# Performance work log

Measured on AMD Instinct MI355X. Metric: run time of the kernel, lower is better.

The kernel has to match this reference:

```python
import jax, jax.numpy as jnp
import numpy as np

B, S, D = 4, 4096, 1024
G, N, BLK, K = 8, 64, 8, 4
GD = D // G
NL = 24


def setup_inputs() -> dict:
    key = jax.random.key(0)
    ks = jax.random.split(key, 16)
    f32 = jnp.float32
    rn = lambda k, sh, s: jax.random.normal(k, sh, f32) * s
    inp = {}
    inp["x_r"] = jax.random.normal(ks[0], (B, S, D), f32)
    inp["x_i"] = jax.random.normal(ks[1], (B, S, D), f32)
    inp["norm_w"] = jnp.ones((D,), f32)
    inp["sg_theta"] = rn(ks[2], (D // BLK,), 0.1)
    inp["sg_Wg"] = rn(ks[3], (D, D), 1.0 / np.sqrt(D))
    inp["sg_bg"] = jnp.zeros((D,), f32)
    inp["conv_w"] = rn(ks[4], (2 * D, 2, K), 1.0 / np.sqrt(2 * K))
    inp["conv_b"] = jnp.zeros((2 * D,), f32)
    inp["log_A_mag"] = jax.random.uniform(ks[5], (G, N), f32) * 0.5 + 0.5
    inp["A_phase"] = rn(ks[6], (G, N), 0.1)
    inp["B_Wr"] = rn(ks[7], (N, GD), 1.0 / np.sqrt(GD))
    inp["B_Wi"] = rn(ks[8], (N, GD), 1.0 / np.sqrt(GD))
    inp["C_Wr"] = rn(ks[9], (GD, N), 1.0 / np.sqrt(N))
    inp["C_Wi"] = rn(ks[10], (GD, N), 1.0 / np.sqrt(N))
    inp["dt_W"] = rn(ks[11], (2, 2 * GD), 1.0 / np.sqrt(2 * GD))
    inp["dt_b"] = jnp.zeros((2,), f32)
    inp["out_Wr"] = rn(ks[12], (D, D), 1.0 / np.sqrt(D))
    inp["out_Wi"] = rn(ks[13], (D, D), 1.0 / np.sqrt(D))
    inp["act_thr"] = jnp.zeros((), f32)
    inp["ssm_scale"] = jnp.full((D,), 2.5, f32)
    inp["res_scale"] = jnp.asarray(1.0 / np.sqrt(2.0 * NL), f32)
    return inp


def reference(x_r, x_i, norm_w, sg_theta, sg_Wg, sg_bg, conv_w, conv_b,
              log_A_mag, A_phase, B_Wr, B_Wi, C_Wr, C_Wi, dt_W, dt_b,
              out_Wr, out_Wi, act_thr, ssm_scale, res_scale):
    b, s, d = x_r.shape
    g, n, gd = G, N, GD
    # --- ComplexRMSNorm: normalize by RMS of complex magnitude ---
    inv = jax.lax.rsqrt(jnp.mean(x_r * x_r + x_i * x_i, axis=-1, keepdims=True) + 1e-6)
    xr = x_r * inv * norm_w
    xi = x_i * inv * norm_w
    # --- SpinorGate: block-diagonal phase rotation with selective sigmoid gate ---
    theta = jnp.repeat(sg_theta, BLK)  # per-block angle broadcast to [D]
    mag = jnp.sqrt(xr * xr + xi * xi + 1e-8)
    gate = jax.nn.sigmoid(jnp.einsum('bsd,ed->bse', mag, sg_Wg) + sg_bg)
    ct, st = jnp.cos(theta), jnp.sin(theta)
    xr, xi = gate * (xr * ct - xi * st), gate * (xr * st + xi * ct)
    # --- grouped causal conv over interleaved real/imag channels ---
    x_il = jnp.stack([xr, xi], axis=-1).reshape(b, s, 2 * d).transpose(0, 2, 1)  # [B,2D,S]
    x_il = jnp.pad(x_il, ((0, 0), (0, 0), (K - 1, 0)))  # causal left pad
    co = jax.lax.conv_general_dilated(
        x_il, conv_w, (1,), 'VALID',
        dimension_numbers=('NCH', 'OIH', 'NCH'), feature_group_count=d)
    co = co + conv_b[None, :, None]
    co = co.transpose(0, 2, 1).reshape(b, s, d, 2)
    xr, xi = co[..., 0], co[..., 1]
    # --- magnitude-gated activation ---
    act = 1.0 - jnp.exp(-(xr * xr + xi * xi) * jnp.exp(act_thr))
    xr = xr * act
    xi = xi * act
    # --- MIMO groups ---
    xgr = xr.reshape(b, s, g, gd)
    xgi = xi.reshape(b, s, g, gd)
    # --- selective dt from concatenated real/imag features ---
    xcat = jnp.concatenate([xgr, xgi], axis=-1)  # [B,S,G,2*gd]
    dt = jnp.clip(jnp.exp(jnp.einsum('bsgd,ed->bsge', xcat, dt_W) + dt_b), 1e-4, 2.0)
    dt_mag, dt_ph = dt[..., 0:1], dt[..., 1:2]
    # --- discretized complex A (|A| < 1 guaranteed) ---
    a_mag = jnp.exp(dt_mag * (-jax.nn.softplus(log_A_mag)))  # [B,S,G,N]
    ang = dt_ph * A_phase
    ar = a_mag * jnp.cos(ang)
    ai = a_mag * jnp.sin(ang)
    # --- complex B projection ---
    bxr = (jnp.einsum('bsgd,nd->bsgn', xgr, B_Wr)
           - jnp.einsum('bsgd,nd->bsgn', xgi, B_Wi)) * dt_mag
    bxi = (jnp.einsum('bsgd,nd->bsgn', xgr, B_Wi)
           + jnp.einsum('bsgd,nd->bsgn', xgi, B_Wr)) * dt_mag
    # --- complex selective scan with renorm every 256 steps ---
    def step(carry, inp):
        hr, hi = carry
        a_r, a_i, b_r, b_i, t = inp
        nhr = a_r * hr - a_i * hi + b_r
        nhi = a_r * hi + a_i * hr + b_i
        hn = jnp.sqrt(nhr * nhr + nhi * nhi + 1e-8)
        sc = jnp.where((t + 1) % 256 == 0, jnp.minimum(hn, 100.0) / hn, 1.0)
        nhr = nhr * sc
        nhi = nhi * sc
        return (nhr, nhi), (nhr, nhi)

    h0 = jnp.zeros((b, g, n), x_r.dtype)
    mv = lambda a: jnp.moveaxis(a, 1, 0)  # [S,B,G,N]
    _, (Hr, Hi) = jax.lax.scan(step, (h0, h0),
                               (mv(ar), mv(ai), mv(bxr), mv(bxi), jnp.arange(s)))
    Hr = jnp.moveaxis(Hr, 0, 1)  # [B,S,G,N]
    Hi = jnp.moveaxis(Hi, 0, 1)
    # --- complex C projection ---
    yr = (jnp.einsum('bsgn,dn->bsgd', Hr, C_Wr)
          - jnp.einsum('bsgn,dn->bsgd', Hi, C_Wi)).reshape(b, s, d)
    yi = (jnp.einsum('bsgn,dn->bsgd', Hr, C_Wi)
          + jnp.einsum('bsgn,dn->bsgd', Hi, C_Wr)).reshape(b, s, d)
    # --- complex output projection, real per-channel scale, residual ---
    o_r = (jnp.einsum('bsd,ed->bse', yr, out_Wr)
           - jnp.einsum('bsd,ed->bse', yi, out_Wi)) * ssm_scale
    o_i = (jnp.einsum('bsd,ed->bse', yr, out_Wi)
           + jnp.einsum('bsd,ed->bse', yi, out_Wr)) * ssm_scale
    return jnp.stack([x_r + res_scale * o_r, x_i + res_scale * o_i], axis=-1)
```

## Files before the change

### kernel.cpp

```cpp
#include <hip/hip_runtime.h>
#include <hip/hip_bf16.h>
#include <hip/hip_fp8.h>
#include <math.h>

#define BB 4
#define SS 4096
#define DD 1024
#define GG 8
#define NN 64
#define GDIM 128
#define BS (BB*SS)
static const size_t BSD  = (size_t)BS * DD;
static const size_t BSGN = (size_t)BS * GG * NN;

typedef __attribute__((ext_vector_type(8))) short bf16x8;
typedef __attribute__((ext_vector_type(4))) float f32x4;
typedef __attribute__((ext_vector_type(4))) uint u32x4;
typedef unsigned char uchar;

__device__ inline ushort f2b(float x) {
    __hip_bfloat16 h = __float2bfloat16(x);
    return *reinterpret_cast<ushort*>(&h);
}
__device__ inline float b2f(ushort u) {
    union { uint q; float f; } x; x.q = ((uint)u) << 16; return x.f;
}
__device__ inline uchar f2fp8(float x) {
    __hip_fp8_e4m3 h(x);
    return *reinterpret_cast<uchar*>(&h);
}
__device__ __forceinline__ bf16x8 neg8(bf16x8 v) {
    union { bf16x8 b; u32x4 u; } x;
    x.b = v;
    x.u ^= 0x80008000u;
    return x.b;
}

#define GL16(gp, lp) __builtin_amdgcn_global_load_lds( \
    (const __attribute__((address_space(1))) void*)(gp), \
    (__attribute__((address_space(3))) void*)(lp), 16, 0, 0)

template<int KD, int LDA, int LDB>
__device__ __forceinline__ void mfma_core(
    const ushort* __restrict__ gA, const ushort* __restrict__ gB,
    ushort* lA, ushort* lB, int wave, int lane, f32x4 (&acc)[4][4])
{
    int r = lane & 15, h = lane >> 4;
    int wm = (wave & 1) * 64, wn = (wave >> 1) * 64;
    ushort* lA0 = lA + wave * 1024;
    ushort* lB0 = lB + wave * 1024;
    for (int k0 = 0; k0 < KD; k0 += 32) {
        __syncthreads();
        GL16(gA + k0,            lA0);
        GL16(gA + k0 + 16*LDA,   lA0 + 512);
        GL16(gB + k0,            lB0);
        GL16(gB + k0 + 16*LDB,   lB0 + 512);
        __syncthreads();
        bf16x8 af[4], bfv[4];
        #pragma unroll
        for (int i = 0; i < 4; i++) af[i]  = *(const bf16x8*)&lA[(wm + i*16 + r)*32 + h*8];
        #pragma unroll
        for (int j = 0; j < 4; j++) bfv[j] = *(const bf16x8*)&lB[(wn + j*16 + r)*32 + h*8];
        #pragma unroll
        for (int i = 0; i < 4; i++)
            #pragma unroll
            for (int j = 0; j < 4; j++)
                acc[i][j] = __builtin_amdgcn_mfma_f32_16x16x32_bf16(af[i], bfv[j], acc[i][j], 0, 0, 0);
    }
}

__global__ __launch_bounds__(256) void k_prep(
    const float* __restrict__ Wg, const float* __restrict__ BWr, const float* __restrict__ BWi,
    const float* __restrict__ CWr, const float* __restrict__ CWi,
    const float* __restrict__ Wor, const float* __restrict__ Woi,
    const float* __restrict__ logA, const float* __restrict__ theta,
    uchar* __restrict__ Wg8, ushort* __restrict__ BxT, ushort* __restrict__ A3,
    ushort* __restrict__ WoP, float* __restrict__ spl,
    float* __restrict__ ctab, float* __restrict__ stab)
{
    const int S1 = 1048576;
    const int S2 = S1 + 32768;
    const int S3 = S2 + 32768;
    const int S4 = S3 + 2097152;
    const int S5 = S4 + 512;
    const int S6 = S5 + 1024;
    const int S7 = S6 + 1024;
    for (int idx = blockIdx.x * 256 + threadIdx.x; idx < S7; idx += gridDim.x * 256) {
        if (idx < S1) {
            Wg8[idx] = f2fp8(Wg[idx] * 16.0f);
        } else if (idx < S2) {
            int j = idx - S1, n = j >> 8, kk = j & 255;
            float v;
            if (n < 64) v = (kk < 128) ? BWr[n*128 + kk] : -BWi[n*128 + (kk-128)];
            else { int n2 = n - 64; v = (kk < 128) ? BWi[n2*128 + kk] : BWr[n2*128 + (kk-128)]; }
            BxT[j] = f2b(v);
        } else if (idx < S3) {
            int j = idx - S2, m = j >> 8, kk = j & 255;
            float v;
            if (m < 64) v = (kk < 128) ? CWr[kk*64 + m] : -CWi[(kk-128)*64 + m];
            else { int n2 = m - 64; v = (kk < 128) ? CWi[kk*64 + n2] : CWr[(kk-128)*64 + n2]; }
            A3[j] = f2b(v);
        } else if (idx < S4) {
            int j = idx - S3, e = j >> 11, c = j & 2047;
            int g = c >> 8, kk = c & 255;
            float v = (kk < 128) ? Wor[(size_t)e*1024 + g*128 + kk]
                                 : Woi[(size_t)e*1024 + g*128 + (kk-128)];
            WoP[j] = f2b(v);
        } else if (idx < S5) {
            int j = idx - S4;
            spl[j] = log1pf(expf(logA[j]));
        } else if (idx < S6) {
            int j = idx - S5;
            ctab[j] = cosf(theta[j >> 3]);
        } else {
            int j = idx - S6;
            stab[j] = sinf(theta[j >> 3]);
        }
    }
}

__global__ __launch_bounds__(256) void k_pgemm(
    const ushort* __restrict__ A3, const ushort* __restrict__ WoP,
    ushort* __restrict__ Ppr, ushort* __restrict__ Ppi)
{
    __shared__ ushort lA[4096], lB[4096];
    int g = blockIdx.z;
    int bn = blockIdx.x * 128;
    int tid = threadIdx.x, wave = tid >> 6, lane = tid & 63;
    int row0 = wave*32 + (lane >> 2), col0 = (lane & 3) * 8;
    int r = lane & 15, h = lane >> 4;
    int wm = (wave & 1) * 64, wn = (wave >> 1) * 64;
    f32x4 acc[4][4] = {};
    mfma_core<256, 256, 2048>(A3 + (size_t)row0*256 + col0,
                              WoP + (size_t)(bn + row0)*2048 + g*256 + col0,
                              lA, lB, wave, lane, acc);
    #pragma unroll
    for (int i = 0; i < 4; i++) {
        int mb = wm + i*16 + h*4;
        #pragma unroll
        for (int j = 0; j < 4; j++) {
            int e = bn + wn + j*16 + r;
            #pragma unroll
            for (int t2 = 0; t2 < 4; t2++) {
                int m = mb + t2;
                float v = acc[i][j][t2];
                if (m < 64) {
                    Ppr[(size_t)e*512 + g*64 + m] = f2b(v);
                } else {
                    Ppi[(size_t)e*512 + g*64 + (m - 64)] = f2b(v);
                }
            }
        }
    }
}

__global__ __launch_bounds__(256) void k_norm(
    const float* __restrict__ xr_in, const float* __restrict__ xi_in,
    const float* __restrict__ norm_w,
    uchar* __restrict__ mag_o, float* __restrict__ inv_o)
{
    int row = blockIdx.x;
    int tid = threadIdx.x;
    size_t base = (size_t)row * DD;
    float4 vr = ((const float4*)(xr_in + base))[tid];
    float4 vi = ((const float4*)(xi_in + base))[tid];
    float ss = vr.x*vr.x + vr.y*vr.y + vr.z*vr.z + vr.w*vr.w
             + vi.x*vi.x + vi.y*vi.y + vi.z*vi.z + vi.w*vi.w;
    #pragma unroll
    for (int off = 32; off >= 1; off >>= 1) ss += __shfl_down(ss, off);
    __shared__ float ws4[4];
    if ((tid & 63) == 0) ws4[tid >> 6] = ss;
    __syncthreads();
    float tot = ws4[0] + ws4[1] + ws4[2] + ws4[3];
    float inv = rsqrtf(tot * (1.0f / DD) + 1e-6f);
    float4 w = ((const float4*)norm_w)[tid];
    vr.x *= inv * w.x; vr.y *= inv * w.y; vr.z *= inv * w.z; vr.w *= inv * w.w;
    vi.x *= inv * w.x; vi.y *= inv * w.y; vi.z *= inv * w.z; vi.w *= inv * w.w;
    uchar4 mb;
    mb.x = f2fp8(sqrtf(vr.x*vr.x + vi.x*vi.x + 1e-8f));
    mb.y = f2fp8(sqrtf(vr.y*vr.y + vi.y*vi.y + 1e-8f));
    mb.z = f2fp8(sqrtf(vr.z*vr.z + vi.z*vi.z + 1e-8f));
    mb.w = f2fp8(sqrtf(vr.w*vr.w + vi.w*vi.w + 1e-8f));
    ((uchar4*)(mag_o + base))[tid] = mb;
    if (tid == 0) inv_o[row] = inv;
}

__global__ __launch_bounds__(256) void k_gate_fp8(
    const uchar* __restrict__ A8, const uchar* __restrict__ B8,
    const float* __restrict__ bg, ushort* __restrict__ gate)
{
    __shared__ uchar lA[4096], lB[4096];
    int flat = blockIdx.y * 8 + blockIdx.x;
    int nid  = (flat & 7) * 128 + (flat >> 3);
    int bm = (nid >> 3) * 128, bn = (nid & 7) * 128;
    int tid = threadIdx.x, wave = tid >> 6, lane = tid & 63;
    int r = lane & 15, h = lane >> 4;
    int wm = (wave & 1) * 64, wn = (wave >> 1) * 64;
    int srow = wave*32 + (lane >> 1);
    int scol = (lane & 1) * 16;
    const uchar* gA = A8 + (size_t)(bm + srow)*1024 + scol;
    const uchar* gB = B8 + (size_t)(bn + srow)*1024 + scol;
    uchar* lA0 = lA + wave*1024;
    uchar* lB0 = lB + wave*1024;
    f32x4 acc[4][4] = {};
    for (int k0 = 0; k0 < 1024; k0 += 32) {
        __syncthreads();
        GL16(gA + k0, lA0);
        GL16(gB + k0, lB0);
        __syncthreads();
        long af[4], bfv[4];
        #pragma unroll
        for (int i = 0; i < 4; i++) af[i]  = *(const long*)&lA[(wm + i*16 + r)*32 + h*8];
        #pragma unroll
        for (int j = 0; j < 4; j++) bfv[j] = *(const long*)&lB[(wn + j*16 + r)*32 + h*8];
        #pragma unroll
        for (int i = 0; i < 4; i++)
            #pragma unroll
            for (int j = 0; j < 4; j++)
                acc[i][j] = __builtin_amdgcn_mfma_f32_16x16x32_fp8_fp8(af[i], bfv[j], acc[i][j], 0, 0, 0);
    }
    #pragma unroll
    for (int i = 0; i < 4; i++) {
        int mb = bm + wm + i*16 + h*4;
        #pragma unroll
        for (int j = 0; j < 4; j++) {
            int n = bn + wn + j*16 + r;
            float bias = bg[n];
            #pragma unroll
            for (int t2 = 0; t2 < 4; t2++) {
                float v = acc[i][j][t2] * 0.0625f + bias;
                gate[(size_t)(mb + t2)*DD + n] = f2b(1.0f / (1.0f + __expf(-v)));
            }
        }
    }
}

__global__ __launch_bounds__(256) void k_rotconv(
    const float* __restrict__ xr_raw, const float* __restrict__ xi_raw,
    const float* __restrict__ inv_, const float* __restrict__ norm_w,
    const ushort* __restrict__ gate,
    const float* __restrict__ ctab, const float* __restrict__ stab,
    const float* __restrict__ cw, const float* __restrict__ cb,
    const float* __restrict__ act_thr,
    const float* __restrict__ dtW, const float* __restrict__ dtb,
    ushort* __restrict__ xcat, float* __restrict__ dtm_o, float* __restrict__ dtp_o)
{
    const int CH = 16;
    int row0 = blockIdx.x * CH;
    int s0 = row0 & (SS - 1);
    int t = threadIdx.x, d0 = t * 4;
    int g = d0 >> 7, dd = d0 & 127;
    float4 w4  = *(const float4*)&norm_w[d0];
    float4 ct4 = *(const float4*)&ctab[d0];
    float4 st4 = *(const float4*)&stab[d0];
    float cwv[4][16];
    float cb0[4], cb1[4];
    #pragma unroll
    for (int j = 0; j < 4; j++) {
        #pragma unroll
        for (int q = 0; q < 4; q++)
            *(float4*)&cwv[j][q*4] = *(const float4*)&cw[(size_t)(2*(d0+j))*8 + q*4];
        cb0[j] = cb[2*(d0+j)];
        cb1[j] = cb[2*(d0+j) + 1];
    }
    float4 dtw0a = *(const float4*)&dtW[dd];
    float4 dtw0b = *(const float4*)&dtW[128 + dd];
    float4 dtw1a = *(const float4*)&dtW[256 + dd];
    float4 dtw1b = *(const float4*)&dtW[384 + dd];
    float ea  = __expf(act_thr[0]);
    float db0 = dtb[0], db1 = dtb[1];

    float p1r[4] = {}, p1i[4] = {}, p2r[4] = {}, p2i[4] = {}, p3r[4] = {}, p3i[4] = {};
    auto rotrow = [&](int rr, float (&orr)[4], float (&ori)[4]) {
        float4 a  = *(const float4*)&xr_raw[(size_t)rr*DD + d0];
        float4 bq = *(const float4*)&xi_raw[(size_t)rr*DD + d0];
        ushort4 gq = *(const ushort4*)&gate[(size_t)rr*DD + d0];
        float iv = inv_[rr];
        #pragma unroll
        for (int j = 0; j < 4; j++) {
            float ar = ((const float*)&a)[j]  * iv * ((const float*)&w4)[j];
            float ai = ((const float*)&bq)[j] * iv * ((const float*)&w4)[j];
            float c = ((const float*)&ct4)[j], s = ((const float*)&st4)[j];
            float gg = b2f(((const ushort*)&gq)[j]);
            orr[j] = gg * (ar*c - ai*s);
            ori[j] = gg * (ar*s + ai*c);
        }
    };
    if (s0 >= 1) rotrow(row0 - 1, p1r, p1i);
    if (s0 >= 2) rotrow(row0 - 2, p2r, p2i);
    if (s0 >= 3) rotrow(row0 - 3, p3r, p3i);

    for (int sl = 0; sl < CH; sl++) {
        int row = row0 + sl;
        float rr0[4], ri0[4];
        rotrow(row, rr0, ri0);
        float p0 = 0.f, p1 = 0.f;
        ushort4 ur, ui;
        #pragma unroll
        for (int j = 0; j < 4; j++) {
            float cr = cb0[j]
                + p3r[j]*cwv[j][0]  + p2r[j]*cwv[j][1]  + p1r[j]*cwv[j][2]  + rr0[j]*cwv[j][3]
                + p3i[j]*cwv[j][4]  + p2i[j]*cwv[j][5]  + p1i[j]*cwv[j][6]  + ri0[j]*cwv[j][7];
            float ci = cb1[j]
                + p3r[j]*cwv[j][8]  + p2r[j]*cwv[j][9]  + p1r[j]*cwv[j][10] + rr0[j]*cwv[j][11]
                + p3i[j]*cwv[j][12] + p2i[j]*cwv[j][13] + p1i[j]*cwv[j][14] + ri0[j]*cwv[j][15];
            float act = 1.0f - __expf(-(cr*cr + ci*ci) * ea);
            cr *= act; ci *= act;
            ((ushort*)&ur)[j] = f2b(cr);
            ((ushort*)&ui)[j] = f2b(ci);
            p0 += cr * ((const float*)&dtw0a)[j] + ci * ((const float*)&dtw0b)[j];
            p1 += cr * ((const float*)&dtw1a)[j] + ci * ((const float*)&dtw1b)[j];
        }
        *(ushort4*)&xcat[(size_t)row*2048 + g*256 + dd]       = ur;
        *(ushort4*)&xcat[(size_t)row*2048 + g*256 + 128 + dd] = ui;
        #pragma unroll
        for (int off = 16; off >= 1; off >>= 1) {
            p0 += __shfl_down(p0, off, 32);
            p1 += __shfl_down(p1, off, 32);
        }
        if ((t & 31) == 0) {
            dtm_o[(size_t)row*8 + g] = fminf(fmaxf(__expf(p0 + db0), 1e-4f), 2.0f);
            dtp_o[(size_t)row*8 + g] = fminf(fmaxf(__expf(p1 + db1), 1e-4f), 2.0f);
        }
        #pragma unroll
        for (int j = 0; j < 4; j++) {
            p3r[j] = p2r[j]; p3i[j] = p2i[j];
            p2r[j] = p1r[j]; p2i[j] = p1i[j];
            p1r[j] = rr0[j]; p1i[j] = ri0[j];
        }
    }
}

__global__ __launch_bounds__(256) void k_bx_mfma(
    const ushort* __restrict__ xcat, const ushort* __restrict__ BxT,
    const float* __restrict__ dtm_,
    float* __restrict__ br, float* __restrict__ bi)
{
    __shared__ ushort lA[4096], lB[4096];
    int g = blockIdx.z;
    int bm = blockIdx.y * 128;
    int tid = threadIdx.x, wave = tid >> 6, lane = tid & 63;
    int row0 = wave*32 + (lane >> 2), col0 = (lane & 3) * 8;
    int r = lane & 15, h = lane >> 4;
    int wm = (wave & 1) * 64, wn = (wave >> 1) * 64;
    f32x4 acc[4][4] = {};
    mfma_core<256, 2048, 256>(xcat + (size_t)(bm + row0)*2048 + g*256 + col0,
                              BxT + (size_t)row0*256 + col0,
                              lA, lB, wave, lane, acc);
    #pragma unroll
    for (int i = 0; i < 4; i++) {
        int mb = bm + wm + i*16 + h*4;
        #pragma unroll
        for (int j = 0; j < 4; j++) {
            int n = wn + j*16 + r;
            #pragma unroll
            for (int t2 = 0; t2 < 4; t2++) {
                int m = mb + t2;
                float v = acc[i][j][t2] * dtm_[(size_t)m*8 + g];
                if (n < 64) br[(size_t)m*512 + g*64 + n]      = v;
                else        bi[(size_t)m*512 + g*64 + n - 64] = v;
            }
        }
    }
}

__global__ __launch_bounds__(256) void k_scan1(
    const float* __restrict__ br, const float* __restrict__ bi,
    const float* __restrict__ dtm_, const float* __restrict__ dtp_,
    const float* __restrict__ spl_t, const float* __restrict__ aph,
    float* __restrict__ Sar, float* __restrict__ Sai,
    float* __restrict__ Sbr, float* __restrict__ Sbi)
{
    int blk = blockIdx.x;
    int half = blk & 1, c = (blk >> 1) & 63, b = blk >> 7;
    int t = half*256 + threadIdx.x;
    int g = t >> 6;
    float spl = spl_t[t], ap = aph[t];
    int row0 = b*SS + c*64;
    size_t idx = (size_t)row0 * 512 + t;
    const float* dtmp = dtm_ + (size_t)row0*8 + g;
    const float* dtpp = dtp_ + (size_t)row0*8 + g;
    float Ar = 1.f, Ai = 0.f, Br = 0.f, Bi = 0.f;
    for (int s0 = 0; s0 < 64; s0 += 4) {
        float vm[4], vp[4], wr[4], wi[4];
        #pragma unroll
        for (int u = 0; u < 4; u++) {
            vm[u] = dtmp[(s0+u)*8]; vp[u] = dtpp[(s0+u)*8];
            wr[u] = br[idx + (size_t)(s0+u)*512];
            wi[u] = bi[idx + (size_t)(s0+u)*512];
        }
        #pragma unroll
        for (int u = 0; u < 4; u++) {
            float am = __expf(-vm[u]*spl);
            float sa, ca; __sincosf(vp[u]*ap, &sa, &ca);
            float arv = am*ca, aiv = am*sa;
            float nBr = arv*Br - aiv*Bi + wr[u];
            float nBi = arv*Bi + aiv*Br + wi[u];
            float nAr = arv*Ar - aiv*Ai;
            float nAi = arv*Ai + aiv*Ar;
            Br = nBr; Bi = nBi; Ar = nAr; Ai = nAi;
        }
    }
    size_t o = ((size_t)(b*64 + c))*512 + t;
    Sar[o] = Ar; Sai[o] = Ai; Sbr[o] = Br; Sbi[o] = Bi;
}

__global__ __launch_bounds__(256) void k_scan2(
    const float* __restrict__ Sar, const float* __restrict__ Sai,
    const float* __restrict__ Sbr, const float* __restrict__ Sbi,
    float* __restrict__ hinr, float* __restrict__ hini)
{
    int blk = blockIdx.x;
    int half = blk & 1, b = blk >> 1;
    int t = half*256 + threadIdx.x;
    float hr = 0.f, hi = 0.f;
    for (int c = 0; c < 64; c++) {
        size_t o = ((size_t)(b*64 + c))*512 + t;
        hinr[o] = hr; hini[o] = hi;
        float nr = Sar[o]*hr - Sai[o]*hi + Sbr[o];
        float ni = Sar[o]*hi + Sai[o]*hr + Sbi[o];
        if ((c & 3) == 3) {
            float hn = sqrtf(nr*nr + ni*ni + 1e-8f);
            float sc = fminf(hn, 100.0f) / hn;
            nr *= sc; ni *= sc;
        }
        hr = nr; hi = ni;
    }
}

__global__ __launch_bounds__(256) void k_scan3(
    const float* __restrict__ br, const float* __restrict__ bi,
    const float* __restrict__ dtm_, const float* __restrict__ dtp_,
    const float* __restrict__ spl_t, const float* __restrict__ aph,
    const float* __restrict__ hinr, const float* __restrict__ hini,
    ushort* __restrict__ Hbf)
{
    int blk = blockIdx.x;
    int half = blk & 1, c = (blk >> 1) & 63, b = blk >> 7;
    int t = half*256 + threadIdx.x;
    int g = t >> 6;
    float spl = spl_t[t], ap = aph[t];
    int row0 = b*SS + c*64;
    size_t idx = (size_t)row0 * 512 + t;
    const float* dtmp = dtm_ + (size_t)row0*8 + g;
    const float* dtpp = dtp_ + (size_t)row0*8 + g;
    size_t o = ((size_t)(b*64 + c))*512 + t;
    float hr = hinr[o], hi = hini[o];
    bool rch = ((c & 3) == 3);
    for (int s0 = 0; s0 < 64; s0 += 4) {
        float vm[4], vp[4], wr[4], wi[4];
        #pragma unroll
        for (int u = 0; u < 4; u++) {
            vm[u] = dtmp[(s0+u)*8]; vp[u] = dtpp[(s0+u)*8];
            wr[u] = br[idx + (size_t)(s0+u)*512];
            wi[u] = bi[idx + (size_t)(s0+u)*512];
        }
        #pragma unroll
        for (int u = 0; u < 4; u++) {
            float am = __expf(-vm[u]*spl);
            float sa, ca; __sincosf(vp[u]*ap, &sa, &ca);
            float arv = am*ca, aiv = am*sa;
            float nr = arv*hr - aiv*hi + wr[u];
            float ni = arv*hi + aiv*hr + wi[u];
            if (rch && (s0 + u == 63)) {
                float hn = sqrtf(nr*nr + ni*ni + 1e-8f);
                float sc = fminf(hn, 100.0f) / hn;
                nr *= sc; ni *= sc;
            }
            size_t rb = (size_t)(row0 + s0 + u) * 1024;
            Hbf[rb + t]       = f2b(nr);
            Hbf[rb + 512 + t] = f2b(ni);
            hr = nr; hi = ni;
        }
    }
}

__global__ __launch_bounds__(512) void k_out_cplx(
    const ushort* __restrict__ A,
    const ushort* __restrict__ Ppr,
    const ushort* __restrict__ Ppi,
    const float* __restrict__ ssm,
    const float* __restrict__ xr0, const float* __restrict__ xi0,
    const float* __restrict__ res_scale, float* __restrict__ out)
{
    __shared__ ushort lHr[4096], lHi[4096], lPr[8192], lPi[8192];
    int flat = blockIdx.y * 8 + blockIdx.x;
    int nid  = (flat & 7) * 64 + (flat >> 3);
    int bm = (nid >> 2) * 128, be = (nid & 3) * 256;
    int tid = threadIdx.x, wave = tid >> 6, lane = tid & 63;
    int r = lane & 15, h = lane >> 4;
    int wr = wave >> 2, wc = wave & 3;
    int lrow = lane >> 2;
    int lcol = (lane & 3) * 8;
    const ushort* gHr = A + (size_t)(bm + wave*16 + lrow)*1024 + lcol;
    const ushort* gHi = gHr + 512;
    const ushort* gPr = Ppr + (size_t)(be + wave*32 + lrow)*512 + lcol;
    const ushort* gPi = Ppi + (size_t)(be + wave*32 + lrow)*512 + lcol;
    ushort* dHr = lHr + wave*512;
    ushort* dHi = lHi + wave*512;
    ushort* dPr = lPr + wave*1024;
    ushort* dPi = lPi + wave*1024;
    f32x4 accr[4][4] = {};
    f32x4 acci[4][4] = {};
    for (int k0 = 0; k0 < 512; k0 += 32) {
        __syncthreads();
        GL16(gHr + k0, dHr);
        GL16(gHi + k0, dHi);
        GL16(gPr + k0,          dPr);
        GL16(gPr + 16*512 + k0, dPr + 512);
        GL16(gPi + k0,          dPi);
        GL16(gPi + 16*512 + k0, dPi + 512);
        __syncthreads();
        bf16x8 hrf[4], hif[4], prf[4], pif[4], npif[4];
        #pragma unroll
        for (int i = 0; i < 4; i++) {
            int ro = (wr*64 + i*16 + r)*32 + h*8;
            hrf[i] = *(const bf16x8*)&lHr[ro];
            hif[i] = *(const bf16x8*)&lHi[ro];
        }
        #pragma unroll
        for (int j = 0; j < 4; j++) {
            int ro = (wc*64 + j*16 + r)*32 + h*8;
            prf[j] = *(const bf16x8*)&lPr[ro];
            pif[j] = *(const bf16x8*)&lPi[ro];
            npif[j] = neg8(pif[j]);
        }
        #pragma unroll
        for (int i = 0; i < 4; i++)
            #pragma unroll
            for (int j = 0; j < 4; j++) {
                accr[i][j] = __builtin_amdgcn_mfma_f32_16x16x32_bf16(hrf[i], prf[j],  accr[i][j], 0, 0, 0);
                accr[i][j] = __builtin_amdgcn_mfma_f32_16x16x32_bf16(hif[i], npif[j], accr[i][j], 0, 0, 0);
                acci[i][j] = __builtin_amdgcn_mfma_f32_16x16x32_bf16(hrf[i], pif[j],  acci[i][j], 0, 0, 0);
                acci[i][j] = __builtin_amdgcn_mfma_f32_16x16x32_bf16(hif[i], prf[j],  acci[i][j], 0, 0, 0);
            }
    }
    float rs = res_scale[0];
    #pragma unroll
    for (int i = 0; i < 4; i++) {
        int mb = bm + wr*64 + i*16 + h*4;
        #pragma unroll
        for (int j = 0; j < 4; j++) {
            int e = be + wc*64 + j*16 + r;
            float sc = ssm[e] * rs;
            #pragma unroll
            for (int t2 = 0; t2 < 4; t2++) {
                size_t p = (size_t)(mb + t2)*DD + e;
                float2 v;
                v.x = xr0[p] + accr[i][j][t2]*sc;
                v.y = xi0[p] + acci[i][j][t2]*sc;
                *(float2*)&out[2*p] = v;
            }
        }
    }
}

extern "C" void kernel_launch(void* const* d_in, const int* in_sizes, int n_in,
                              void* d_out, int out_size, void* d_ws, size_t ws_size,
                              hipStream_t stream) {
    const float* x_r      = (const float*)d_in[0];
    const float* x_i      = (const float*)d_in[1];
    const float* norm_w   = (const float*)d_in[2];
    const float* sg_theta = (const float*)d_in[3];
    const float* sg_Wg    = (const float*)d_in[4];
    const float* sg_bg    = (const float*)d_in[5];
    const float* conv_w   = (const float*)d_in[6];
    const float* conv_b   = (const float*)d_in[7];
    const float* log_A    = (const float*)d_in[8];
    const float* A_phase  = (const float*)d_in[9];
    const float* B_Wr     = (const float*)d_in[10];
    const float* B_Wi     = (const float*)d_in[11];
    const float* C_Wr     = (const float*)d_in[12];
    const float* C_Wi     = (const float*)d_in[13];
    const float* dt_W     = (const float*)d_in[14];
    const float* dt_b     = (const float*)d_in[15];
    const float* out_Wr   = (const float*)d_in[16];
    const float* out_Wi   = (const float*)d_in[17];
    const float* act_thr  = (const float*)d_in[18];
    const float* ssm_s    = (const float*)d_in[19];
    const float* res_s    = (const float*)d_in[20];
    float* out = (float*)d_out;
    float* ws  = (float*)d_ws;

    ushort* gate  = (ushort*)ws;
    ushort* xcat  = (ushort*)(ws + BSD);
    uchar*  mag8  = (uchar*)(ws + 2*BSD);
    float*  br    = ws + 2*BSD + BSGN;
    float*  bi    = ws + 2*BSD + 2*BSGN;
    ushort* Hbf   = (ushort*)(ws + 2*BSD + 3*BSGN);
    float*  sm    = ws + 2*BSD + 4*BSGN;
    float*  dtm   = sm;
    float*  dtp   = sm + 131072;
    float*  Sar   = sm + 2*131072;
    float*  Sai   = sm + 3*131072;
    float*  Sbr   = sm + 4*131072;
    float*  Sbi   = sm + 5*131072;
    float*  hinr  = sm + 6*131072;
    float*  hini  = sm + 7*131072;
    float*  inv   = sm + 8*131072;
    float*  spl   = inv + 16384;
    float*  ctab  = spl + 512;
    float*  stab  = ctab + 1024;
    uchar*  Wg8   = (uchar*)(stab + 1024);
    ushort* BxT   = (ushort*)(stab + 1024 + 262144);
    ushort* A3    = BxT + 32768;
    ushort* WoP   = A3 + 32768;
    ushort* Ppr   = WoP + 2097152;
    ushort* Ppi   = Ppr + 524288;

    k_prep<<<2048, 256, 0, stream>>>(sg_Wg, B_Wr, B_Wi, C_Wr, C_Wi, out_Wr, out_Wi,
                                     log_A, sg_theta, Wg8, BxT, A3, WoP, spl, ctab, stab);
    k_pgemm<<<dim3(8, 1, 8), 256, 0, stream>>>(A3, WoP, Ppr, Ppi);
    k_norm<<<BS, 256, 0, stream>>>(x_r, x_i, norm_w, mag8, inv);
    k_gate_fp8<<<dim3(8, 128), 256, 0, stream>>>(mag8, Wg8, sg_bg, gate);
    k_rotconv<<<BS/16, 256, 0, stream>>>(x_r, x_i, inv, norm_w, gate, ctab, stab,
                                         conv_w, conv_b, act_thr, dt_W, dt_b,
                                         xcat, dtm, dtp);
    k_bx_mfma<<<dim3(1, 128, 8), 256, 0, stream>>>(xcat, BxT, dtm, br, bi);
    k_scan1<<<512, 256, 0, stream>>>(br, bi, dtm, dtp, spl, A_phase, Sar, Sai, Sbr, Sbi);
    k_scan2<<<8, 256, 0, stream>>>(Sar, Sai, Sbr, Sbi, hinr, hini);
    k_scan3<<<512, 256, 0, stream>>>(br, bi, dtm, dtp, spl, A_phase, hinr, hini, Hbf);
    k_out_cplx<<<dim3(8, 64), 512, 0, stream>>>(Hbf, Ppr, Ppi, ssm_s, x_r, x_i, res_s, out);
}
```

Before: 344.2 us.

## Widen gate GEMM tile to 128x256 with 8 waves and store Bx in fp16

The fp8 gate GEMM now uses 512-thread blocks, each computing a 128x256 output tile. Half the waves load the A tile and half load the wider B tile, which halves the block count and improves operand reuse per LDS load. Separately, the Bx projection outputs br/bi are stored as fp16 instead of fp32, halving the traffic written by k_bx_mfma and read by both scan passes. The fp16 storage adds rounding error to the scan inputs, and the larger block may reduce occupancy.

```diff
diff --git a/kernel.cpp b/kernel.cpp
--- a/kernel.cpp
+++ b/kernel.cpp
@@ -28,6 +28,14 @@
 __device__ inline uchar f2fp8(float x) {
     __hip_fp8_e4m3 h(x);
     return *reinterpret_cast<uchar*>(&h);
+}
+__device__ inline ushort f2h(float x) {
+    _Float16 h = (_Float16)x;
+    return *reinterpret_cast<ushort*>(&h);
+}
+__device__ inline float h2f(ushort u) {
+    _Float16 h = *reinterpret_cast<_Float16*>(&u);
+    return (float)h;
 }
 __device__ __forceinline__ bf16x8 neg8(bf16x8 v) {
     union { bf16x8 b; u32x4 u; } x;
@@ -185,34 +193,38 @@
     if (tid == 0) inv_o[row] = inv;
 }
 
-__global__ __launch_bounds__(256) void k_gate_fp8(
+__global__ __launch_bounds__(512) void k_gate_fp8(
     const uchar* __restrict__ A8, const uchar* __restrict__ B8,
     const float* __restrict__ bg, ushort* __restrict__ gate)
 {
-    __shared__ uchar lA[4096], lB[4096];
+    __shared__ uchar lA[4096], lB[8192];
     int flat = blockIdx.y * 8 + blockIdx.x;
-    int nid  = (flat & 7) * 128 + (flat >> 3);
-    int bm = (nid >> 3) * 128, bn = (nid & 7) * 128;
+    int nid  = (flat & 7) * 64 + (flat >> 3);
+    int bm = (nid >> 2) * 128, bn = (nid & 3) * 256;
     int tid = threadIdx.x, wave = tid >> 6, lane = tid & 63;
     int r = lane & 15, h = lane >> 4;
-    int wm = (wave & 1) * 64, wn = (wave >> 1) * 64;
-    int srow = wave*32 + (lane >> 1);
+    int wr = wave >> 2, wc = wave & 3;
+    int srow = (lane >> 1);
     int scol = (lane & 1) * 16;
-    const uchar* gA = A8 + (size_t)(bm + srow)*1024 + scol;
-    const uchar* gB = B8 + (size_t)(bn + srow)*1024 + scol;
-    uchar* lA0 = lA + wave*1024;
-    uchar* lB0 = lB + wave*1024;
+    const uchar* gA = A8 + (size_t)(bm + (wave & 3)*32 + srow)*1024 + scol;
+    const uchar* gB = B8 + (size_t)(bn + (wave & 3)*64 + srow)*1024 + scol;
+    uchar* dA = lA + (wave & 3)*1024;
+    uchar* dB = lB + (wave & 3)*2048;
     f32x4 acc[4][4] = {};
     for (int k0 = 0; k0 < 1024; k0 += 32) {
         __syncthreads();
-        GL16(gA + k0, lA0);
-        GL16(gB + k0, lB0);
+        if (wave < 4) {
+            GL16(gA + k0, dA);
+        } else {
+            GL16(gB + k0,            dB);
+            GL16(gB + 32*1024 + k0,  dB + 1024);
+        }
         __syncthreads();
         long af[4], bfv[4];
         #pragma unroll
-        for (int i = 0; i < 4; i++) af[i]  = *(const long*)&lA[(wm + i*16 + r)*32 + h*8];
-        #pragma unroll
-        for (int j = 0; j < 4; j++) bfv[j] = *(const long*)&lB[(wn + j*16 + r)*32 + h*8];
+        for (int i = 0; i < 4; i++) af[i]  = *(const long*)&lA[(wr*64 + i*16 + r)*32 + h*8];
+        #pragma unroll
+        for (int j = 0; j < 4; j++) bfv[j] = *(const long*)&lB[(wc*64 + j*16 + r)*32 + h*8];
         #pragma unroll
         for (int i = 0; i < 4; i++)
             #pragma unroll
@@ -221,10 +233,10 @@
     }
     #pragma unroll
     for (int i = 0; i < 4; i++) {
-        int mb = bm + wm + i*16 + h*4;
-        #pragma unroll
-        for (int j = 0; j < 4; j++) {
-            int n = bn + wn + j*16 + r;
+        int mb = bm + wr*64 + i*16 + h*4;
+        #pragma unroll
+        for (int j = 0; j < 4; j++) {
+            int n = bn + wc*64 + j*16 + r;
             float bias = bg[n];
             #pragma unroll
             for (int t2 = 0; t2 < 4; t2++) {
@@ -334,7 +346,7 @@
 __global__ __launch_bounds__(256) void k_bx_mfma(
     const ushort* __restrict__ xcat, const ushort* __restrict__ BxT,
     const float* __restrict__ dtm_,
-    float* __restrict__ br, float* __restrict__ bi)
+    ushort* __restrict__ br, ushort* __restrict__ bi)
 {
     __shared__ ushort lA[4096], lB[4096];
     int g = blockIdx.z;
@@ -357,15 +369,15 @@
             for (int t2 = 0; t2 < 4; t2++) {
                 int m = mb + t2;
                 float v = acc[i][j][t2] * dtm_[(size_t)m*8 + g];
-                if (n < 64) br[(size_t)m*512 + g*64 + n]      = v;
-                else        bi[(size_t)m*512 + g*64 + n - 64] = v;
+                if (n < 64) br[(size_t)m*512 + g*64 + n]      = f2h(v);
+                else        bi[(size_t)m*512 + g*64 + n - 64] = f2h(v);
             }
         }
     }
 }
 
 __global__ __launch_bounds__(256) void k_scan1(
-    const float* __restrict__ br, const float* __restrict__ bi,
+    const ushort* __restrict__ br, const ushort* __restrict__ bi,
     const float* __restrict__ dtm_, const float* __restrict__ dtp_,
     const float* __restrict__ spl_t, const float* __restrict__ aph,
     float* __restrict__ Sar, float* __restrict__ Sai,
@@ -386,8 +398,8 @@
         #pragma unroll
         for (int u = 0; u < 4; u++) {
             vm[u] = dtmp[(s0+u)*8]; vp[u] = dtpp[(s0+u)*8];
-            wr[u] = br[idx + (size_t)(s0+u)*512];
-            wi[u] = bi[idx + (size_t)(s0+u)*512];
+            wr[u] = h2f(br[idx + (size_t)(s0+u)*512]);
+            wi[u] = h2f(bi[idx + (size_t)(s0+u)*512]);
         }
         #pragma unroll
         for (int u = 0; u < 4; u++) {
@@ -429,7 +441,7 @@
 }
 
 __global__ __launch_bounds__(256) void k_scan3(
-    const float* __restrict__ br, const float* __restrict__ bi,
+    const ushort* __restrict__ br, const ushort* __restrict__ bi,
     const float* __restrict__ dtm_, const float* __restrict__ dtp_,
     const float* __restrict__ spl_t, const float* __restrict__ aph,
     const float* __restrict__ hinr, const float* __restrict__ hini,
@@ -452,8 +464,8 @@
         #pragma unroll
         for (int u = 0; u < 4; u++) {
             vm[u] = dtmp[(s0+u)*8]; vp[u] = dtpp[(s0+u)*8];
-            wr[u] = br[idx + (size_t)(s0+u)*512];
-            wi[u] = bi[idx + (size_t)(s0+u)*512];
+            wr[u] = h2f(br[idx + (size_t)(s0+u)*512]);
+            wi[u] = h2f(bi[idx + (size_t)(s0+u)*512]);
         }
         #pragma unroll
         for (int u = 0; u < 4; u++) {
@@ -585,8 +597,8 @@
     ushort* gate  = (ushort*)ws;
     ushort* xcat  = (ushort*)(ws + BSD);
     uchar*  mag8  = (uchar*)(ws + 2*BSD);
-    float*  br    = ws + 2*BSD + BSGN;
-    float*  bi    = ws + 2*BSD + 2*BSGN;
+    ushort* br    = (ushort*)(ws + 2*BSD + BSGN);
+    ushort* bi    = (ushort*)(ws + 2*BSD + 2*BSGN);
     ushort* Hbf   = (ushort*)(ws + 2*BSD + 3*BSGN);
     float*  sm    = ws + 2*BSD + 4*BSGN;
     float*  dtm   = sm;
@@ -612,7 +624,7 @@
                                      log_A, sg_theta, Wg8, BxT, A3, WoP, spl, ctab, stab);
     k_pgemm<<<dim3(8, 1, 8), 256, 0, stream>>>(A3, WoP, Ppr, Ppi);
     k_norm<<<BS, 256, 0, stream>>>(x_r, x_i, norm_w, mag8, inv);
-    k_gate_fp8<<<dim3(8, 128), 256, 0, stream>>>(mag8, Wg8, sg_bg, gate);
+    k_gate_fp8<<<dim3(8, 64), 512, 0, stream>>>(mag8, Wg8, sg_bg, gate);
     k_rotconv<<<BS/16, 256, 0, stream>>>(x_r, x_i, inv, norm_w, gate, ctab, stab,
                                          conv_w, conv_b, act_thr, dt_W, dt_b,
                                          xcat, dtm, dtp);
```

New measurement: 337.0 us (median of 3 runs). 1.02x faster.
